# Kernel tuning notes

Hardware: AMD Instinct MI355X
Metric: run time of the kernel (lower is better)

## Reference

```python
import jax, jax.numpy as jnp
import numpy as np

B, L, D = 32, 512, 1024

def setup_inputs() -> dict:
    key = jax.random.key(0)
    ks = jax.random.split(key, 9)
    s = 0.02
    return {
        "query": jax.random.normal(ks[0], (B, L, D), jnp.float32),
        "context": jax.random.normal(ks[1], (B, L, D), jnp.float32),
        "W_in": jax.random.normal(ks[2], (D, D), jnp.float32) * s,
        "b_in": jax.random.normal(ks[3], (D,), jnp.float32) * s,
        "W_in2": jax.random.normal(ks[4], (D, D), jnp.float32) * s,
        "b_in2": jax.random.normal(ks[5], (D,), jnp.float32) * s,
        "W_out": jax.random.normal(ks[6], (L, D), jnp.float32) * s,  # windows_lens == L
        "W_fc": jax.random.normal(ks[7], (D, 2 * D), jnp.float32) * s,
        "b_fc": jax.random.normal(ks[8], (D,), jnp.float32) * s,
    }

def reference(query, context, W_in, b_in, W_in2, b_in2, W_out, W_fc, b_fc):
    # additive (Bahdanau) score: tanh(Wq q + Wc c) @ W_out^T -> [B, L, L]
    q = jnp.einsum('bld,ed->ble', query, W_in) + b_in
    c = jnp.einsum('bld,ed->ble', context, W_in2) + b_in2
    alpha = jnp.einsum('bld,wd->blw', jnp.tanh(q + c), W_out)  # [B, L, L]
    alpha = jax.nn.softmax(alpha, axis=-1)
    mix = jnp.einsum('blw,bwd->bld', alpha, context)           # bmm
    cat = jnp.concatenate([mix, context], axis=-1)             # [B, L, 2D]
    out = jnp.einsum('blf,df->bld', cat, W_fc) + b_fc
    return out, alpha
```

## Files before the change

kernel.cpp:

```cpp
#include <hip/hip_runtime.h>
#include <hip/hip_bf16.h>
#include <cstdint>

typedef unsigned short u16;
typedef unsigned int u32;
typedef __bf16 bf16x8 __attribute__((ext_vector_type(8)));
typedef float f32x4 __attribute__((ext_vector_type(4)));
typedef u16 u16x8 __attribute__((ext_vector_type(8)));

#define DEVINL __device__ __forceinline__

typedef __attribute__((address_space(1))) const u32 gbl_u32;
typedef __attribute__((address_space(3))) u32 lds_u32;

DEVINL void llds16(const void* g, void* l) {
  __builtin_amdgcn_global_load_lds((gbl_u32*)g, (lds_u32*)l, 16, 0, 0);
}

DEVINL u16 f2bf(float f) {
  union { float f; u32 i; } x; x.f = f;
  u32 r = x.i + 0x7FFFu + ((x.i >> 16) & 1u);
  return (u16)(r >> 16);
}

DEVINL float fast_tanh(float x) {
  x = fminf(10.f, fmaxf(-10.f, x));
  float e = __expf(2.f * x);
  return (e - 1.f) / (e + 1.f);
}

DEVINL bf16x8 cvt8(const float4& a, const float4& b) {
  bf16x8 r;
  r[0] = (__bf16)a.x; r[1] = (__bf16)a.y; r[2] = (__bf16)a.z; r[3] = (__bf16)a.w;
  r[4] = (__bf16)b.x; r[5] = (__bf16)b.y; r[6] = (__bf16)b.z; r[7] = (__bf16)b.w;
  return r;
}

__global__ __launch_bounds__(256) void cvtk(const float* __restrict__ src,
                                            u16* __restrict__ dst, int n8) {
  int i = blockIdx.x * 256 + threadIdx.x;
  if (i >= n8) return;
  const float* s = src + (size_t)i * 8;
  *(bf16x8*)(dst + (size_t)i * 8) = cvt8(*(const float4*)s, *(const float4*)(s + 4));
}

__global__ __launch_bounds__(256) void tile_b(const float* __restrict__ src,
                                              int srcld, int koff,
                                              u16* __restrict__ dst, int nchunks) {
  int id = blockIdx.x * 256 + threadIdx.x;
  if (id >= nchunks) return;
  int n = id >> 7, k8 = id & 127;
  int kb = k8 >> 2, h = k8 & 3;
  int u = h * 128 + ((n & 127) ^ (h << 1));
  const float* s = src + (size_t)n * srcld + koff + k8 * 8;
  size_t dc = ((size_t)((n >> 7) * 32 + kb) * 512 + u) * 8;
  *(bf16x8*)(dst + dc) = cvt8(*(const float4*)s, *(const float4*)(s + 4));
}

__global__ __launch_bounds__(256) void tile_b64(const float* __restrict__ src,
                                                int srcld, int koff,
                                                u16* __restrict__ dst, int nchunks) {
  int id = blockIdx.x * 256 + threadIdx.x;
  if (id >= nchunks) return;
  int n = id >> 7, k8 = id & 127;
  int kb = k8 >> 3, h = k8 & 7;
  int u = h * 256 + ((n & 255) ^ (h << 1));
  const float* s = src + (size_t)n * srcld + koff + k8 * 8;
  size_t dc = ((size_t)((n >> 8) * 16 + kb) * 2048 + u) * 8;
  *(bf16x8*)(dst + dc) = cvt8(*(const float4*)s, *(const float4*)(s + 4));
}

template <int NSEG, bool OUT_BF16, bool TANH>
__global__ __launch_bounds__(512) void gemm_nt7(
    const u16* __restrict__ A0, const u16* __restrict__ A1,
    const u16* __restrict__ Bt0, const u16* __restrict__ Bt1,
    const float* __restrict__ bias0, const float* __restrict__ bias1,
    void* __restrict__ Cout, int ldc) {
  __shared__ u16 As[2][16384];
  __shared__ u16 Bs[2][16384];
  const int tid = threadIdx.x, lane = tid & 63, w = tid >> 6;
  const int wr = w >> 2, wc = w & 3;

  const int NX = gridDim.x;
  const int total = NX * gridDim.y;
  const int flat = blockIdx.y * NX + blockIdx.x;
  const int wid = (flat & 7) * (total >> 3) + (flat >> 3);
  const int nb = wid % NX;
  const int n0 = nb * 256, m0 = (wid / NX) * 256;

  f32x4 acc[8][4];
#pragma unroll
  for (int i = 0; i < 8; ++i)
#pragma unroll
    for (int j = 0; j < 4; ++j) acc[i][j] = (f32x4)0.f;

  u32 asrc[4], bofs[4];
#pragma unroll
  for (int r = 0; r < 4; ++r) {
    int u = r * 512 + w * 64 + lane;
    int row = u >> 3, oct = (u & 7) ^ (row & 7);
    asrc[r] = (u32)(m0 + row) * 1024u + (u32)(oct * 8);
    bofs[r] = (u32)u * 8u;
  }

  const int NT = NSEG * 16;

  auto stage = [&](int t, int buf) {
    const int seg = (NSEG == 2 && t >= 16) ? 1 : 0;
    const int kb = t - (seg << 4);
    const u16* Ap = seg ? A1 : A0;
    const u16* Bt = (seg ? Bt1 : Bt0) + ((size_t)(nb * 16 + kb) << 14);
    const u32 k0 = (u32)(kb << 6);
#pragma unroll
    for (int r = 0; r < 4; ++r) {
      llds16(Ap + (size_t)(asrc[r] + k0), &As[buf][(r * 512 + w * 64) * 8]);
      llds16(Bt + (size_t)bofs[r], &Bs[buf][(r * 512 + w * 64) * 8]);
    }
  };
  auto compute = [&](int buf) {
    const int rl = lane & 15;
#pragma unroll
    for (int kh = 0; kh < 2; ++kh) {
      const int h = kh * 4 + (lane >> 4);
      const int jA = h ^ (rl & 7);
      const int rlxB = rl ^ (h << 1);
      const int hbB = h * 256;
      bf16x8 af[8], bv[4];
#pragma unroll
      for (int i = 0; i < 8; ++i)
        af[i] = *(const bf16x8*)&As[buf][((wr * 128 + i * 16 + rl) * 8 + jA) * 8];
#pragma unroll
      for (int j = 0; j < 4; ++j)
        bv[j] = *(const bf16x8*)&Bs[buf][(hbB + ((wc * 64 + j * 16) ^ 0) + rlxB) * 8
                                         + ((wc * 64 + j * 16 + rl) ^ (h << 1)) * 0];
#pragma unroll
      for (int j = 0; j < 4; ++j)
        bv[j] = *(const bf16x8*)&Bs[buf][(hbB + ((wc * 64 + j * 16 + rl) ^ (h << 1))) * 8];
#pragma unroll
      for (int i = 0; i < 8; ++i)
#pragma unroll
        for (int j = 0; j < 4; ++j)
          acc[i][j] =
              __builtin_amdgcn_mfma_f32_16x16x32_bf16(af[i], bv[j], acc[i][j], 0, 0, 0);
    }
  };

  stage(0, 0);
  for (int t = 0; t < NT; ++t) {
    const int c = t & 1;
    if (t + 1 < NT) {
      stage(t + 1, c ^ 1);
      asm volatile("s_waitcnt vmcnt(8)" ::: "memory");
    } else {
      asm volatile("s_waitcnt vmcnt(0)" ::: "memory");
    }
    __builtin_amdgcn_s_barrier();
    __builtin_amdgcn_sched_barrier(0);
    compute(c);
    __builtin_amdgcn_s_barrier();
  }

  const int rl = lane & 15, rq = lane >> 4;
#pragma unroll
  for (int j = 0; j < 4; ++j) {
    const int gc = n0 + wc * 64 + j * 16 + rl;
    float bia = 0.f;
    if (bias0) bia += bias0[gc];
    if (NSEG == 2 && bias1) bia += bias1[gc];
#pragma unroll
    for (int i = 0; i < 8; ++i) {
#pragma unroll
      for (int r = 0; r < 4; ++r) {
        const int grow = m0 + wr * 128 + i * 16 + rq * 4 + r;
        float v = acc[i][j][r] + bia;
        if (TANH) v = fast_tanh(v);
        if (OUT_BF16)
          ((u16*)Cout)[(size_t)grow * ldc + gc] = f2bf(v);
        else
          ((float*)Cout)[(size_t)grow * ldc + gc] = v;
      }
    }
  }
}

template <int NSEG, bool OUT_BF16, bool TANH>
__global__ __launch_bounds__(256) void gemm_nt4(
    const u16* __restrict__ A0, const u16* __restrict__ A1, int lda,
    const u16* __restrict__ Bt0, const u16* __restrict__ Bt1,
    const float* __restrict__ bias0, const float* __restrict__ bias1,
    void* __restrict__ Cout, int ldc) {
  __shared__ u16 As[2][4096];
  __shared__ u16 Bs[2][4096];
  const int tid = threadIdx.x, lane = tid & 63, w = tid >> 6;
  const int wr = w >> 1, wc = w & 1;
  const int NX = gridDim.x;
  const int total = NX * gridDim.y;
  const int flat = blockIdx.y * NX + blockIdx.x;
  const int wid = (flat & 7) * (total >> 3) + (flat >> 3);
  const int nb = wid % NX;
  const int n0 = nb * 128, m0 = (wid / NX) * 128;
  const int h = lane >> 4, rl = lane & 15;
  const int rlx = rl ^ (h << 1);
  const int jA = h ^ (rl & 3);

  f32x4 acc[4][4];
#pragma unroll
  for (int i = 0; i < 4; ++i)
#pragma unroll
    for (int j = 0; j < 4; ++j) acc[i][j] = (f32x4)0.f;

  const int gb0 = w * 64, gb1 = 256 + w * 64;
  u32 asrc[2];
  {
    int u0 = gb0 + lane, u1 = gb1 + lane;
    int r0 = u0 >> 2, o0 = (u0 & 3) ^ (r0 & 3);
    int r1 = u1 >> 2, o1 = (u1 & 3) ^ (r1 & 3);
    asrc[0] = (u32)(m0 + r0) * (u32)lda + (u32)(o0 * 8);
    asrc[1] = (u32)(m0 + r1) * (u32)lda + (u32)(o1 * 8);
  }
  const int NT = NSEG * 32;

  auto stage = [&](int t, int buf) {
    const int seg = (NSEG == 2 && t >= 32) ? 1 : 0;
    const int kb = t - seg * 32, kl = kb << 5;
    {
      const u16* Bt = (seg ? Bt1 : Bt0) + ((size_t)(nb * 32 + kb) * 512) * 8;
      llds16(Bt + (size_t)(gb0 + lane) * 8, &Bs[buf][gb0 * 8]);
      llds16(Bt + (size_t)(gb1 + lane) * 8, &Bs[buf][gb1 * 8]);
    }
    {
      const u16* Ap = seg ? A1 : A0;
      llds16(Ap + (size_t)(asrc[0] + kl), &As[buf][gb0 * 8]);
      llds16(Ap + (size_t)(asrc[1] + kl), &As[buf][gb1 * 8]);
    }
  };
  auto compute = [&](int buf) {
    bf16x8 af[4], bfv[4];
#pragma unroll
    for (int i = 0; i < 4; ++i)
      af[i] = *(const bf16x8*)&As[buf][((wr * 64 + i * 16 + rl) * 4 + jA) * 8];
#pragma unroll
    for (int j = 0; j < 4; ++j)
      bfv[j] = *(const bf16x8*)&Bs[buf][(h * 128 + ((wc * 64 + j * 16 + rl) ^ (h << 1))) * 8];
#pragma unroll
    for (int i = 0; i < 4; ++i)
#pragma unroll
      for (int j = 0; j < 4; ++j)
        acc[i][j] =
            __builtin_amdgcn_mfma_f32_16x16x32_bf16(af[i], bfv[j], acc[i][j], 0, 0, 0);
  };

  stage(0, 0);
  for (int t = 0; t < NT; ++t) {
    const int c = t & 1;
    if (t + 1 < NT) {
      stage(t + 1, c ^ 1);
      asm volatile("s_waitcnt vmcnt(4)" ::: "memory");
    } else {
      asm volatile("s_waitcnt vmcnt(0)" ::: "memory");
    }
    __builtin_amdgcn_s_barrier();
    __builtin_amdgcn_sched_barrier(0);
    compute(c);
    __builtin_amdgcn_s_barrier();
  }

  const int rq = lane >> 4;
#pragma unroll
  for (int j = 0; j < 4; ++j) {
    const int gc = n0 + wc * 64 + j * 16 + rl;
    float bia = 0.f;
    if (bias0) bia += bias0[gc];
    if (NSEG == 2 && bias1) bia += bias1[gc];
#pragma unroll
    for (int i = 0; i < 4; ++i) {
#pragma unroll
      for (int r = 0; r < 4; ++r) {
        const int grow = m0 + wr * 64 + i * 16 + rq * 4 + r;
        float v = acc[i][j][r] + bia;
        if (TANH) v = fast_tanh(v);
        if (OUT_BF16)
          ((u16*)Cout)[(size_t)grow * ldc + gc] = f2bf(v);
        else
          ((float*)Cout)[(size_t)grow * ldc + gc] = v;
      }
    }
  }
}

__global__ __launch_bounds__(256) void gemm_nn3(
    const float* __restrict__ alpha, const u16* __restrict__ ctxb,
    u16* __restrict__ mix) {
  __shared__ u16 As[2][4096];
  __shared__ u16 Bs[2][4096];
  const int tid = threadIdx.x, lane = tid & 63, w = tid >> 6;
  const int wr = w >> 1, wc = w & 1;
  const int b = blockIdx.z;
  const int n0 = blockIdx.x * 128, m0 = blockIdx.y * 128;
  const int h = lane >> 4, rlx = (lane & 15) ^ (h << 1);
  const float* A = alpha + (size_t)b * 262144;
  u16* C = mix + (size_t)b * 524288;

  f32x4 acc[4][4];
#pragma unroll
  for (int i = 0; i < 4; ++i)
#pragma unroll
    for (int j = 0; j < 4; ++j) acc[i][j] = (f32x4)0.f;

  const int row0 = tid >> 2, cb = tid & 3, row1 = 64 + row0;
  const int unit0 = cb * 128 + (row0 ^ (cb << 1));
  const int unit1 = cb * 128 + (row1 ^ (cb << 1));
  const int kl = tid & 31, ng = tid >> 5;
  const int hb = kl >> 3, kp = kl & 7;

  float4 fr[4];
  u16x8 ub[2];

  auto stage = [&](int t) {
    const int k0 = t << 5;
    const float* p0 = A + (size_t)(m0 + row0) * 512 + k0 + cb * 8;
    const float* p1 = A + (size_t)(m0 + row1) * 512 + k0 + cb * 8;
    fr[0] = *(const float4*)p0; fr[1] = *(const float4*)(p0 + 4);
    fr[2] = *(const float4*)p1; fr[3] = *(const float4*)(p1 + 4);
    const u16* Cb = ctxb + (size_t)b * 524288 + (size_t)(k0 + kl) * 1024 +
                    n0 + ng * 16;
    ub[0] = *(const u16x8*)Cb; ub[1] = *(const u16x8*)(Cb + 8);
  };
  auto stage_fin = [&](int buf) {
    *(bf16x8*)&As[buf][unit0 * 8] = cvt8(fr[0], fr[1]);
    *(bf16x8*)&As[buf][unit1 * 8] = cvt8(fr[2], fr[3]);
#pragma unroll
    for (int j = 0; j < 16; ++j) {
      int n = ng * 16 + j;
      Bs[buf][(hb * 128 + (n ^ (hb << 1))) * 8 + kp] =
          (j < 8) ? ub[0][j] : ub[1][j - 8];
    }
  };
  auto compute = [&](int buf) {
    bf16x8 af[4], bfv[4];
#pragma unroll
    for (int i = 0; i < 4; ++i)
      af[i] = *(const bf16x8*)&As[buf][(h * 128 + wr * 64 + i * 16 + rlx) * 8];
#pragma unroll
    for (int j = 0; j < 4; ++j)
      bfv[j] = *(const bf16x8*)&Bs[buf][(h * 128 + wc * 64 + j * 16 + rlx) * 8];
#pragma unroll
    for (int i = 0; i < 4; ++i)
#pragma unroll
      for (int j = 0; j < 4; ++j)
        acc[i][j] =
            __builtin_amdgcn_mfma_f32_16x16x32_bf16(af[i], bfv[j], acc[i][j], 0, 0, 0);
  };

  stage(0);
  stage_fin(0);
  __syncthreads();
  for (int t = 0; t < 16; ++t) {
    const int cb_ = t & 1;
    if (t + 1 < 16) stage(t + 1);
    compute(cb_);
    if (t + 1 < 16) stage_fin(cb_ ^ 1);
    __syncthreads();
  }

  const int rl = lane & 15, rq = lane >> 4;
#pragma unroll
  for (int j = 0; j < 4; ++j) {
    const int gc = n0 + wc * 64 + j * 16 + rl;
#pragma unroll
    for (int i = 0; i < 4; ++i) {
#pragma unroll
      for (int r = 0; r < 4; ++r) {
        const int grow = m0 + wr * 64 + i * 16 + rq * 4 + r;
        C[(size_t)grow * 1024 + gc] = f2bf(acc[i][j][r]);
      }
    }
  }
}

__global__ __launch_bounds__(256) void softmax_rows_f32(float* __restrict__ S) {
  const int row = blockIdx.x * 4 + (threadIdx.x >> 6);
  const int lane = threadIdx.x & 63;
  float* s = S + (size_t)row * 512 + lane * 8;
  float4 v0 = *(const float4*)s;
  float4 v1 = *(const float4*)(s + 4);
  float vs[8] = {v0.x, v0.y, v0.z, v0.w, v1.x, v1.y, v1.z, v1.w};
  float vm = vs[0];
#pragma unroll
  for (int j = 1; j < 8; ++j) vm = fmaxf(vm, vs[j]);
#pragma unroll
  for (int off = 32; off > 0; off >>= 1) vm = fmaxf(vm, __shfl_xor(vm, off, 64));
  float e[8];
  float sum = 0.f;
#pragma unroll
  for (int j = 0; j < 8; ++j) { e[j] = __expf(vs[j] - vm); sum += e[j]; }
#pragma unroll
  for (int off = 32; off > 0; off >>= 1) sum += __shfl_xor(sum, off, 64);
  float inv = 1.f / sum;
  float4 o0 = {e[0] * inv, e[1] * inv, e[2] * inv, e[3] * inv};
  float4 o1 = {e[4] * inv, e[5] * inv, e[6] * inv, e[7] * inv};
  *(float4*)s = o0;
  *(float4*)(s + 4) = o1;
}

extern "C" void kernel_launch(void* const* d_in, const int* in_sizes, int n_in,
                              void* d_out, int out_size, void* d_ws, size_t ws_size,
                              hipStream_t stream) {
  const float* query = (const float*)d_in[0];
  const float* ctx   = (const float*)d_in[1];
  const float* W_in  = (const float*)d_in[2];
  const float* b_in  = (const float*)d_in[3];
  const float* W_in2 = (const float*)d_in[4];
  const float* b_in2 = (const float*)d_in[5];
  const float* W_out = (const float*)d_in[6];
  const float* W_fc  = (const float*)d_in[7];
  const float* b_fc  = (const float*)d_in[8];

  float* out   = (float*)d_out;
  float* alpha = (float*)d_out + 16777216;

  u16* wibf_t  = (u16*)d_ws;
  u16* wi2bf_t = wibf_t + 1048576;
  u16* wobf_t  = wibf_t + 2097152;
  u16* wf0_t   = wibf_t + 2621440;
  u16* wf1_t   = wibf_t + 3670016;
  u16* t_ws    = (u16*)((char*)d_ws + 9437184);
  u16* cbf     = (u16*)((char*)d_ws + 42991616);
  u16* qbf     = (u16*)((char*)d_ws + 76546048);

  dim3 blk(256, 1, 1);
  dim3 blk5(512, 1, 1);

  tile_b64<<<dim3(512), blk, 0, stream>>>(W_in, 1024, 0, wibf_t, 131072);
  tile_b64<<<dim3(512), blk, 0, stream>>>(W_in2, 1024, 0, wi2bf_t, 131072);
  tile_b<<<dim3(256), blk, 0, stream>>>(W_out, 1024, 0, wobf_t, 65536);
  tile_b64<<<dim3(512), blk, 0, stream>>>(W_fc, 2048, 0, wf0_t, 131072);
  tile_b64<<<dim3(512), blk, 0, stream>>>(W_fc, 2048, 1024, wf1_t, 131072);
  cvtk<<<dim3(8192), blk, 0, stream>>>(ctx, cbf, 2097152);
  cvtk<<<dim3(8192), blk, 0, stream>>>(query, qbf, 2097152);

  gemm_nt7<2, true, true><<<dim3(4, 64), blk5, 0, stream>>>(
      qbf, cbf, wibf_t, wi2bf_t, b_in, b_in2, t_ws, 1024);

  gemm_nt4<1, false, false><<<dim3(4, 128), blk, 0, stream>>>(
      t_ws, nullptr, 1024, wobf_t, nullptr, nullptr, nullptr, alpha, 512);

  softmax_rows_f32<<<dim3(4096), blk, 0, stream>>>(alpha);

  gemm_nn3<<<dim3(8, 4, 32), blk, 0, stream>>>(alpha, cbf, t_ws);

  gemm_nt7<2, false, false><<<dim3(4, 64), blk5, 0, stream>>>(
      t_ws, cbf, wf0_t, wf1_t, b_fc, nullptr, out, 1024);
}
```

Before: 302.1 us.

## Interleave next-tile global-to-LDS loads with MFMA phases in 256x256 GEMM

Restructures the main loop of the large NT GEMM kernel so the next tile's global_load_lds issues are split into four chunks, each interleaved between half-k MFMA groups, instead of being issued all at once before compute. Each MFMA block is wrapped in s_setprio(1), and barriers plus finer vmcnt waits are used between phases. The goal is to spread memory traffic across the compute so loads overlap MFMA work, in the style of a ping-pong schedule. The cost is more barriers per iteration, and the partial vmcnt accounting needs to stay correct.

```diff
diff --git a/kernel.cpp b/kernel.cpp
--- a/kernel.cpp
+++ b/kernel.cpp
@@ -71,7 +71,7 @@
 }
 
 template <int NSEG, bool OUT_BF16, bool TANH>
-__global__ __launch_bounds__(512) void gemm_nt7(
+__global__ __launch_bounds__(512) void gemm_nt8(
     const u16* __restrict__ A0, const u16* __restrict__ A1,
     const u16* __restrict__ Bt0, const u16* __restrict__ Bt1,
     const float* __restrict__ bias0, const float* __restrict__ bias1,
@@ -105,62 +105,78 @@
 
   const int NT = NSEG * 16;
 
-  auto stage = [&](int t, int buf) {
+  auto stageA = [&](int t, int q) {
     const int seg = (NSEG == 2 && t >= 16) ? 1 : 0;
     const int kb = t - (seg << 4);
     const u16* Ap = seg ? A1 : A0;
+    llds16(Ap + (size_t)(asrc[q] + (u32)(kb << 6)),
+           &As[t & 1][(q * 512 + w * 64) * 8]);
+  };
+  auto stageB = [&](int t, int q) {
+    const int seg = (NSEG == 2 && t >= 16) ? 1 : 0;
+    const int kb = t - (seg << 4);
     const u16* Bt = (seg ? Bt1 : Bt0) + ((size_t)(nb * 16 + kb) << 14);
-    const u32 k0 = (u32)(kb << 6);
-#pragma unroll
-    for (int r = 0; r < 4; ++r) {
-      llds16(Ap + (size_t)(asrc[r] + k0), &As[buf][(r * 512 + w * 64) * 8]);
-      llds16(Bt + (size_t)bofs[r], &Bs[buf][(r * 512 + w * 64) * 8]);
-    }
-  };
-  auto compute = [&](int buf) {
-    const int rl = lane & 15;
+    llds16(Bt + (size_t)bofs[q], &Bs[t & 1][(q * 512 + w * 64) * 8]);
+  };
+
+  stageA(0, 0); stageA(0, 1); stageA(0, 2); stageA(0, 3);
+  stageB(0, 0); stageB(0, 1); stageB(0, 2); stageB(0, 3);
+  asm volatile("s_waitcnt vmcnt(2)" ::: "memory");
+  __builtin_amdgcn_s_barrier();
+
+  const int rl = lane & 15;
+  for (int t = 0; t < NT; ++t) {
+    const int buf = t & 1;
+    const bool pre = (t + 1 < NT);
+
 #pragma unroll
     for (int kh = 0; kh < 2; ++kh) {
       const int h = kh * 4 + (lane >> 4);
       const int jA = h ^ (rl & 7);
-      const int rlxB = rl ^ (h << 1);
-      const int hbB = h * 256;
-      bf16x8 af[8], bv[4];
+      bf16x8 af[8], b0, b1, b2, b3;
 #pragma unroll
       for (int i = 0; i < 8; ++i)
         af[i] = *(const bf16x8*)&As[buf][((wr * 128 + i * 16 + rl) * 8 + jA) * 8];
-#pragma unroll
-      for (int j = 0; j < 4; ++j)
-        bv[j] = *(const bf16x8*)&Bs[buf][(hbB + ((wc * 64 + j * 16) ^ 0) + rlxB) * 8
-                                         + ((wc * 64 + j * 16 + rl) ^ (h << 1)) * 0];
-#pragma unroll
-      for (int j = 0; j < 4; ++j)
-        bv[j] = *(const bf16x8*)&Bs[buf][(hbB + ((wc * 64 + j * 16 + rl) ^ (h << 1))) * 8];
-#pragma unroll
-      for (int i = 0; i < 8; ++i)
-#pragma unroll
-        for (int j = 0; j < 4; ++j)
-          acc[i][j] =
-              __builtin_amdgcn_mfma_f32_16x16x32_bf16(af[i], bv[j], acc[i][j], 0, 0, 0);
-    }
-  };
-
-  stage(0, 0);
-  for (int t = 0; t < NT; ++t) {
-    const int c = t & 1;
-    if (t + 1 < NT) {
-      stage(t + 1, c ^ 1);
-      asm volatile("s_waitcnt vmcnt(8)" ::: "memory");
-    } else {
-      asm volatile("s_waitcnt vmcnt(0)" ::: "memory");
-    }
-    __builtin_amdgcn_s_barrier();
-    __builtin_amdgcn_sched_barrier(0);
-    compute(c);
-    __builtin_amdgcn_s_barrier();
-  }
-
-  const int rl = lane & 15, rq = lane >> 4;
+      b0 = *(const bf16x8*)&Bs[buf][(h * 256 + ((wc * 64 + 0 + rl) ^ (h << 1))) * 8];
+      b1 = *(const bf16x8*)&Bs[buf][(h * 256 + ((wc * 64 + 16 + rl) ^ (h << 1))) * 8];
+      if (pre) {
+        if (kh == 0) { stageA(t + 1, 0); stageA(t + 1, 1); }
+        else         { stageB(t + 1, 0); stageB(t + 1, 1); }
+      }
+      __builtin_amdgcn_s_barrier();
+      __builtin_amdgcn_s_setprio(1);
+#pragma unroll
+      for (int i = 0; i < 8; ++i) {
+        acc[i][0] = __builtin_amdgcn_mfma_f32_16x16x32_bf16(af[i], b0, acc[i][0], 0, 0, 0);
+        acc[i][1] = __builtin_amdgcn_mfma_f32_16x16x32_bf16(af[i], b1, acc[i][1], 0, 0, 0);
+      }
+      __builtin_amdgcn_s_setprio(0);
+      __builtin_amdgcn_s_barrier();
+      b2 = *(const bf16x8*)&Bs[buf][(h * 256 + ((wc * 64 + 32 + rl) ^ (h << 1))) * 8];
+      b3 = *(const bf16x8*)&Bs[buf][(h * 256 + ((wc * 64 + 48 + rl) ^ (h << 1))) * 8];
+      if (pre) {
+        if (kh == 0) { stageA(t + 1, 2); stageA(t + 1, 3); }
+        else         { stageB(t + 1, 2); stageB(t + 1, 3); }
+      }
+      if (kh == 0)
+        asm volatile("s_waitcnt vmcnt(4)" ::: "memory");
+      else if (pre)
+        asm volatile("s_waitcnt vmcnt(2)" ::: "memory");
+      else
+        asm volatile("s_waitcnt vmcnt(0)" ::: "memory");
+      __builtin_amdgcn_s_barrier();
+      __builtin_amdgcn_s_setprio(1);
+#pragma unroll
+      for (int i = 0; i < 8; ++i) {
+        acc[i][2] = __builtin_amdgcn_mfma_f32_16x16x32_bf16(af[i], b2, acc[i][2], 0, 0, 0);
+        acc[i][3] = __builtin_amdgcn_mfma_f32_16x16x32_bf16(af[i], b3, acc[i][3], 0, 0, 0);
+      }
+      __builtin_amdgcn_s_setprio(0);
+      __builtin_amdgcn_s_barrier();
+    }
+  }
+
+  const int rq = lane >> 4;
 #pragma unroll
   for (int j = 0; j < 4; ++j) {
     const int gc = n0 + wc * 64 + j * 16 + rl;
@@ -200,7 +216,6 @@
   const int nb = wid % NX;
   const int n0 = nb * 128, m0 = (wid / NX) * 128;
   const int h = lane >> 4, rl = lane & 15;
-  const int rlx = rl ^ (h << 1);
   const int jA = h ^ (rl & 3);
 
   f32x4 acc[4][4];
@@ -439,7 +454,7 @@
   cvtk<<<dim3(8192), blk, 0, stream>>>(ctx, cbf, 2097152);
   cvtk<<<dim3(8192), blk, 0, stream>>>(query, qbf, 2097152);
 
-  gemm_nt7<2, true, true><<<dim3(4, 64), blk5, 0, stream>>>(
+  gemm_nt8<2, true, true><<<dim3(4, 64), blk5, 0, stream>>>(
       qbf, cbf, wibf_t, wi2bf_t, b_in, b_in2, t_ws, 1024);
 
   gemm_nt4<1, false, false><<<dim3(4, 128), blk, 0, stream>>>(
@@ -449,6 +464,6 @@
 
   gemm_nn3<<<dim3(8, 4, 32), blk, 0, stream>>>(alpha, cbf, t_ws);
 
-  gemm_nt7<2, false, false><<<dim3(4, 64), blk5, 0, stream>>>(
+  gemm_nt8<2, false, false><<<dim3(4, 64), blk5, 0, stream>>>(
       t_ws, cbf, wf0_t, wf1_t, b_fc, nullptr, out, 1024);
 }
```

New measurement: 288.9 us. 4.4% less time.

## Triple-buffer A tiles and split loads across k-halves in the big GEMM

Applied to the files above, without the earlier changes.

Restructures the 256x256 GEMM main loop so A uses three LDS buffers and B two. The prefetch of B for the next step is issued between the two k-halves of compute, and A two steps ahead, with finer vmcnt waits. This removes the trailing barrier per iteration and interleaves global-to-LDS loads with MFMA work. It also raises wave priority around the MFMA blocks. LDS use grows to 160KB per block, which may limit occupancy and depends on the vmcnt counts being exactly right.

```diff
diff --git a/kernel.cpp b/kernel.cpp
--- a/kernel.cpp
+++ b/kernel.cpp
@@ -71,12 +71,12 @@
 }
 
 template <int NSEG, bool OUT_BF16, bool TANH>
-__global__ __launch_bounds__(512) void gemm_nt7(
+__global__ __launch_bounds__(512) void gemm_nt9(
     const u16* __restrict__ A0, const u16* __restrict__ A1,
     const u16* __restrict__ Bt0, const u16* __restrict__ Bt1,
     const float* __restrict__ bias0, const float* __restrict__ bias1,
     void* __restrict__ Cout, int ldc) {
-  __shared__ u16 As[2][16384];
+  __shared__ u16 As[3][16384];
   __shared__ u16 Bs[2][16384];
   const int tid = threadIdx.x, lane = tid & 63, w = tid >> 6;
   const int wr = w >> 2, wc = w & 3;
@@ -105,62 +105,87 @@
 
   const int NT = NSEG * 16;
 
-  auto stage = [&](int t, int buf) {
+  auto stageA = [&](int t) {
     const int seg = (NSEG == 2 && t >= 16) ? 1 : 0;
     const int kb = t - (seg << 4);
     const u16* Ap = seg ? A1 : A0;
+    const u32 k0 = (u32)(kb << 6);
+    u16* dst = As[t % 3];
+#pragma unroll
+    for (int q = 0; q < 4; ++q)
+      llds16(Ap + (size_t)(asrc[q] + k0), dst + (q * 512 + w * 64) * 8);
+  };
+  auto stageB = [&](int t) {
+    const int seg = (NSEG == 2 && t >= 16) ? 1 : 0;
+    const int kb = t - (seg << 4);
     const u16* Bt = (seg ? Bt1 : Bt0) + ((size_t)(nb * 16 + kb) << 14);
-    const u32 k0 = (u32)(kb << 6);
-#pragma unroll
-    for (int r = 0; r < 4; ++r) {
-      llds16(Ap + (size_t)(asrc[r] + k0), &As[buf][(r * 512 + w * 64) * 8]);
-      llds16(Bt + (size_t)bofs[r], &Bs[buf][(r * 512 + w * 64) * 8]);
-    }
-  };
-  auto compute = [&](int buf) {
-    const int rl = lane & 15;
-#pragma unroll
-    for (int kh = 0; kh < 2; ++kh) {
-      const int h = kh * 4 + (lane >> 4);
+    u16* dst = Bs[t & 1];
+#pragma unroll
+    for (int q = 0; q < 4; ++q)
+      llds16(Bt + (size_t)bofs[q], dst + (q * 512 + w * 64) * 8);
+  };
+
+  stageA(0);
+  stageB(0);
+  if (NT > 1) stageA(1);
+
+  const int rl = lane & 15;
+  for (int t = 0; t < NT; ++t) {
+    const int ab = t % 3, bb = t & 1;
+    const bool preB = (t + 1 < NT);
+    const bool preA = (t + 2 < NT);
+
+    if (preB) asm volatile("s_waitcnt vmcnt(6)" ::: "memory");
+    else      asm volatile("s_waitcnt vmcnt(2)" ::: "memory");
+    __builtin_amdgcn_s_barrier();
+    __builtin_amdgcn_sched_barrier(0);
+    {
+      const int h = lane >> 4;
       const int jA = h ^ (rl & 7);
-      const int rlxB = rl ^ (h << 1);
-      const int hbB = h * 256;
       bf16x8 af[8], bv[4];
 #pragma unroll
       for (int i = 0; i < 8; ++i)
-        af[i] = *(const bf16x8*)&As[buf][((wr * 128 + i * 16 + rl) * 8 + jA) * 8];
+        af[i] = *(const bf16x8*)&As[ab][((wr * 128 + i * 16 + rl) * 8 + jA) * 8];
 #pragma unroll
       for (int j = 0; j < 4; ++j)
-        bv[j] = *(const bf16x8*)&Bs[buf][(hbB + ((wc * 64 + j * 16) ^ 0) + rlxB) * 8
-                                         + ((wc * 64 + j * 16 + rl) ^ (h << 1)) * 0];
-#pragma unroll
-      for (int j = 0; j < 4; ++j)
-        bv[j] = *(const bf16x8*)&Bs[buf][(hbB + ((wc * 64 + j * 16 + rl) ^ (h << 1))) * 8];
+        bv[j] = *(const bf16x8*)&Bs[bb][(h * 256 + ((wc * 64 + j * 16 + rl) ^ (h << 1))) * 8];
+      if (preB) stageB(t + 1);
+      __builtin_amdgcn_s_setprio(1);
 #pragma unroll
       for (int i = 0; i < 8; ++i)
 #pragma unroll
         for (int j = 0; j < 4; ++j)
           acc[i][j] =
               __builtin_amdgcn_mfma_f32_16x16x32_bf16(af[i], bv[j], acc[i][j], 0, 0, 0);
-    }
-  };
-
-  stage(0, 0);
-  for (int t = 0; t < NT; ++t) {
-    const int c = t & 1;
-    if (t + 1 < NT) {
-      stage(t + 1, c ^ 1);
-      asm volatile("s_waitcnt vmcnt(8)" ::: "memory");
-    } else {
-      asm volatile("s_waitcnt vmcnt(0)" ::: "memory");
-    }
+      __builtin_amdgcn_s_setprio(0);
+    }
+    if (preB) asm volatile("s_waitcnt vmcnt(8)" ::: "memory");
+    else      asm volatile("s_waitcnt vmcnt(0)" ::: "memory");
     __builtin_amdgcn_s_barrier();
     __builtin_amdgcn_sched_barrier(0);
-    compute(c);
-    __builtin_amdgcn_s_barrier();
-  }
-
-  const int rl = lane & 15, rq = lane >> 4;
+    {
+      const int h = 4 + (lane >> 4);
+      const int jA = h ^ (rl & 7);
+      bf16x8 af[8], bv[4];
+#pragma unroll
+      for (int i = 0; i < 8; ++i)
+        af[i] = *(const bf16x8*)&As[ab][((wr * 128 + i * 16 + rl) * 8 + jA) * 8];
+#pragma unroll
+      for (int j = 0; j < 4; ++j)
+        bv[j] = *(const bf16x8*)&Bs[bb][(h * 256 + ((wc * 64 + j * 16 + rl) ^ (h << 1))) * 8];
+      if (preA) stageA(t + 2);
+      __builtin_amdgcn_s_setprio(1);
+#pragma unroll
+      for (int i = 0; i < 8; ++i)
+#pragma unroll
+        for (int j = 0; j < 4; ++j)
+          acc[i][j] =
+              __builtin_amdgcn_mfma_f32_16x16x32_bf16(af[i], bv[j], acc[i][j], 0, 0, 0);
+      __builtin_amdgcn_s_setprio(0);
+    }
+  }
+
+  const int rq = lane >> 4;
 #pragma unroll
   for (int j = 0; j < 4; ++j) {
     const int gc = n0 + wc * 64 + j * 16 + rl;
@@ -200,7 +225,6 @@
   const int nb = wid % NX;
   const int n0 = nb * 128, m0 = (wid / NX) * 128;
   const int h = lane >> 4, rl = lane & 15;
-  const int rlx = rl ^ (h << 1);
   const int jA = h ^ (rl & 3);
 
   f32x4 acc[4][4];
@@ -439,7 +463,7 @@
   cvtk<<<dim3(8192), blk, 0, stream>>>(ctx, cbf, 2097152);
   cvtk<<<dim3(8192), blk, 0, stream>>>(query, qbf, 2097152);
 
-  gemm_nt7<2, true, true><<<dim3(4, 64), blk5, 0, stream>>>(
+  gemm_nt9<2, true, true><<<dim3(4, 64), blk5, 0, stream>>>(
       qbf, cbf, wibf_t, wi2bf_t, b_in, b_in2, t_ws, 1024);
 
   gemm_nt4<1, false, false><<<dim3(4, 128), blk, 0, stream>>>(
@@ -449,6 +473,6 @@
 
   gemm_nn3<<<dim3(8, 4, 32), blk, 0, stream>>>(alpha, cbf, t_ws);
 
-  gemm_nt7<2, false, false><<<dim3(4, 64), blk5, 0, stream>>>(
+  gemm_nt9<2, false, false><<<dim3(4, 64), blk5, 0, stream>>>(
       t_ws, cbf, wf0_t, wf1_t, b_fc, nullptr, out, 1024);
 }
```

Result: faster. 285.9 us (-5.4%).

## Shrink big NT GEMM tiles to 128x128 with 256 threads and row-swizzled B layout

Applied to the files above, without the earlier changes.

Replaces the 256x256-tile, 512-thread NT GEMM used for the input projection and output FC with a 128x128-tile, 256-thread variant. The grid grows from 256 to 1024 blocks, and the weight-tiling kernel switches B to a row-major XOR-swizzled layout matching the A layout. The aim is better occupancy and load balance across CUs, since 256 blocks under-fill the GPU, and lower LDS per block. The cost is less data reuse per tile, so more global/L2 traffic and a lower MFMA-to-load ratio.

```diff
diff --git a/kernel.cpp b/kernel.cpp
--- a/kernel.cpp
+++ b/kernel.cpp
@@ -57,50 +57,50 @@
   *(bf16x8*)(dst + dc) = cvt8(*(const float4*)s, *(const float4*)(s + 4));
 }
 
-__global__ __launch_bounds__(256) void tile_b64(const float* __restrict__ src,
-                                                int srcld, int koff,
-                                                u16* __restrict__ dst, int nchunks) {
+__global__ __launch_bounds__(256) void tile_bw(const float* __restrict__ src,
+                                               int srcld, int koff,
+                                               u16* __restrict__ dst, int nchunks) {
   int id = blockIdx.x * 256 + threadIdx.x;
   if (id >= nchunks) return;
   int n = id >> 7, k8 = id & 127;
   int kb = k8 >> 3, h = k8 & 7;
-  int u = h * 256 + ((n & 255) ^ (h << 1));
+  int row = n & 127;
+  int u = row * 8 + (h ^ (row & 7));
   const float* s = src + (size_t)n * srcld + koff + k8 * 8;
-  size_t dc = ((size_t)((n >> 8) * 16 + kb) * 2048 + u) * 8;
+  size_t dc = ((size_t)((n >> 7) * 16 + kb) * 1024 + u) * 8;
   *(bf16x8*)(dst + dc) = cvt8(*(const float4*)s, *(const float4*)(s + 4));
 }
 
 template <int NSEG, bool OUT_BF16, bool TANH>
-__global__ __launch_bounds__(512) void gemm_nt7(
+__global__ __launch_bounds__(256) void gemm_nt11(
     const u16* __restrict__ A0, const u16* __restrict__ A1,
     const u16* __restrict__ Bt0, const u16* __restrict__ Bt1,
     const float* __restrict__ bias0, const float* __restrict__ bias1,
     void* __restrict__ Cout, int ldc) {
-  __shared__ u16 As[2][16384];
-  __shared__ u16 Bs[2][16384];
+  __shared__ u16 As[2][8192];
+  __shared__ u16 Bs[2][8192];
   const int tid = threadIdx.x, lane = tid & 63, w = tid >> 6;
-  const int wr = w >> 2, wc = w & 3;
+  const int wr = w >> 1, wc = w & 1;
 
   const int NX = gridDim.x;
   const int total = NX * gridDim.y;
   const int flat = blockIdx.y * NX + blockIdx.x;
   const int wid = (flat & 7) * (total >> 3) + (flat >> 3);
   const int nb = wid % NX;
-  const int n0 = nb * 256, m0 = (wid / NX) * 256;
-
-  f32x4 acc[8][4];
-#pragma unroll
-  for (int i = 0; i < 8; ++i)
+  const int n0 = nb * 128, m0 = (wid / NX) * 128;
+
+  f32x4 acc[4][4];
+#pragma unroll
+  for (int i = 0; i < 4; ++i)
 #pragma unroll
     for (int j = 0; j < 4; ++j) acc[i][j] = (f32x4)0.f;
 
-  u32 asrc[4], bofs[4];
-#pragma unroll
-  for (int r = 0; r < 4; ++r) {
-    int u = r * 512 + w * 64 + lane;
+  u32 asrc[4];
+#pragma unroll
+  for (int q = 0; q < 4; ++q) {
+    int u = q * 256 + tid;
     int row = u >> 3, oct = (u & 7) ^ (row & 7);
-    asrc[r] = (u32)(m0 + row) * 1024u + (u32)(oct * 8);
-    bofs[r] = (u32)u * 8u;
+    asrc[q] = (u32)(m0 + row) * 1024u + (u32)(oct * 8);
   }
 
   const int NT = NSEG * 16;
@@ -109,12 +109,13 @@
     const int seg = (NSEG == 2 && t >= 16) ? 1 : 0;
     const int kb = t - (seg << 4);
     const u16* Ap = seg ? A1 : A0;
-    const u16* Bt = (seg ? Bt1 : Bt0) + ((size_t)(nb * 16 + kb) << 14);
+    const u16* Bt = (seg ? Bt1 : Bt0) + ((size_t)(nb * 16 + kb) << 10) * 8;
     const u32 k0 = (u32)(kb << 6);
 #pragma unroll
-    for (int r = 0; r < 4; ++r) {
-      llds16(Ap + (size_t)(asrc[r] + k0), &As[buf][(r * 512 + w * 64) * 8]);
-      llds16(Bt + (size_t)bofs[r], &Bs[buf][(r * 512 + w * 64) * 8]);
+    for (int q = 0; q < 4; ++q) {
+      llds16(Ap + (size_t)(asrc[q] + k0), &As[buf][(q * 256 + w * 64) * 8]);
+      llds16(Bt + (size_t)(q * 256 + w * 64 + lane) * 8,
+             &Bs[buf][(q * 256 + w * 64) * 8]);
     }
   };
   auto compute = [&](int buf) {
@@ -122,22 +123,16 @@
 #pragma unroll
     for (int kh = 0; kh < 2; ++kh) {
       const int h = kh * 4 + (lane >> 4);
-      const int jA = h ^ (rl & 7);
-      const int rlxB = rl ^ (h << 1);
-      const int hbB = h * 256;
-      bf16x8 af[8], bv[4];
-#pragma unroll
-      for (int i = 0; i < 8; ++i)
-        af[i] = *(const bf16x8*)&As[buf][((wr * 128 + i * 16 + rl) * 8 + jA) * 8];
+      const int sl = h ^ (rl & 7);
+      bf16x8 af[4], bv[4];
+#pragma unroll
+      for (int i = 0; i < 4; ++i)
+        af[i] = *(const bf16x8*)&As[buf][((wr * 64 + i * 16 + rl) * 8 + sl) * 8];
 #pragma unroll
       for (int j = 0; j < 4; ++j)
-        bv[j] = *(const bf16x8*)&Bs[buf][(hbB + ((wc * 64 + j * 16) ^ 0) + rlxB) * 8
-                                         + ((wc * 64 + j * 16 + rl) ^ (h << 1)) * 0];
-#pragma unroll
-      for (int j = 0; j < 4; ++j)
-        bv[j] = *(const bf16x8*)&Bs[buf][(hbB + ((wc * 64 + j * 16 + rl) ^ (h << 1))) * 8];
-#pragma unroll
-      for (int i = 0; i < 8; ++i)
+        bv[j] = *(const bf16x8*)&Bs[buf][((wc * 64 + j * 16 + rl) * 8 + sl) * 8];
+#pragma unroll
+      for (int i = 0; i < 4; ++i)
 #pragma unroll
         for (int j = 0; j < 4; ++j)
           acc[i][j] =
@@ -168,10 +163,10 @@
     if (bias0) bia += bias0[gc];
     if (NSEG == 2 && bias1) bia += bias1[gc];
 #pragma unroll
-    for (int i = 0; i < 8; ++i) {
+    for (int i = 0; i < 4; ++i) {
 #pragma unroll
       for (int r = 0; r < 4; ++r) {
-        const int grow = m0 + wr * 128 + i * 16 + rq * 4 + r;
+        const int grow = m0 + wr * 64 + i * 16 + rq * 4 + r;
         float v = acc[i][j][r] + bia;
         if (TANH) v = fast_tanh(v);
         if (OUT_BF16)
@@ -200,7 +195,6 @@
   const int nb = wid % NX;
   const int n0 = nb * 128, m0 = (wid / NX) * 128;
   const int h = lane >> 4, rl = lane & 15;
-  const int rlx = rl ^ (h << 1);
   const int jA = h ^ (rl & 3);
 
   f32x4 acc[4][4];
@@ -429,17 +423,16 @@
   u16* qbf     = (u16*)((char*)d_ws + 76546048);
 
   dim3 blk(256, 1, 1);
-  dim3 blk5(512, 1, 1);
-
-  tile_b64<<<dim3(512), blk, 0, stream>>>(W_in, 1024, 0, wibf_t, 131072);
-  tile_b64<<<dim3(512), blk, 0, stream>>>(W_in2, 1024, 0, wi2bf_t, 131072);
+
+  tile_bw<<<dim3(512), blk, 0, stream>>>(W_in, 1024, 0, wibf_t, 131072);
+  tile_bw<<<dim3(512), blk, 0, stream>>>(W_in2, 1024, 0, wi2bf_t, 131072);
   tile_b<<<dim3(256), blk, 0, stream>>>(W_out, 1024, 0, wobf_t, 65536);
-  tile_b64<<<dim3(512), blk, 0, stream>>>(W_fc, 2048, 0, wf0_t, 131072);
-  tile_b64<<<dim3(512), blk, 0, stream>>>(W_fc, 2048, 1024, wf1_t, 131072);
+  tile_bw<<<dim3(512), blk, 0, stream>>>(W_fc, 2048, 0, wf0_t, 131072);
+  tile_bw<<<dim3(512), blk, 0, stream>>>(W_fc, 2048, 1024, wf1_t, 131072);
   cvtk<<<dim3(8192), blk, 0, stream>>>(ctx, cbf, 2097152);
   cvtk<<<dim3(8192), blk, 0, stream>>>(query, qbf, 2097152);
 
-  gemm_nt7<2, true, true><<<dim3(4, 64), blk5, 0, stream>>>(
+  gemm_nt11<2, true, true><<<dim3(8, 128), blk, 0, stream>>>(
       qbf, cbf, wibf_t, wi2bf_t, b_in, b_in2, t_ws, 1024);
 
   gemm_nt4<1, false, false><<<dim3(4, 128), blk, 0, stream>>>(
@@ -449,6 +442,6 @@
 
   gemm_nn3<<<dim3(8, 4, 32), blk, 0, stream>>>(alpha, cbf, t_ws);
 
-  gemm_nt7<2, false, false><<<dim3(4, 64), blk5, 0, stream>>>(
+  gemm_nt11<2, false, false><<<dim3(8, 128), blk, 0, stream>>>(
       t_ws, cbf, wf0_t, wf1_t, b_fc, nullptr, out, 1024);
 }
```

New measurement: 303.4 us. No clear change (+0.4%).
